# Kernel tuning notes

Hardware: AMD Instinct MI355X
Metric: run time of the kernel (lower is better)

## Reference

```python
import jax, jax.numpy as jnp
import numpy as np

R_DIM = 32
D_DIM = 64
N_AGENTS = 16
BATCH = 65536  # num_samples * N_AGENTS = 4096 * 16


def setup_inputs() -> dict:
    key = jax.random.key(0)
    kx, kl, kq, kk, kv, ko = jax.random.split(key, 6)
    x = jax.random.normal(kx, (BATCH, D_DIM, N_AGENTS), dtype=jnp.float32)
    L = jax.random.randint(kl, (BATCH, N_AGENTS, N_AGENTS), 0, 2).astype(jnp.float32)
    Aq = 0.5 * jax.random.normal(kq, (R_DIM, D_DIM), dtype=jnp.float32)
    Ak = 0.5 * jax.random.normal(kk, (R_DIM, D_DIM), dtype=jnp.float32)
    Av = 0.5 * jax.random.normal(kv, (R_DIM, D_DIM), dtype=jnp.float32)
    Ao = 0.5 * jax.random.normal(ko, (1, R_DIM), dtype=jnp.float32)
    return {"x": x, "L": L, "Aq": Aq, "Ak": Ak, "Av": Av, "Ao": Ao}


def reference(x, L, Aq, Ak, Av, Ao):
    B, d, n = x.shape
    S = B // n  # number of samples (x stacks n agents per sample)
    # numNeighbors: count of entries >= 1 in first row of L, plus 1 -> [B,1,1]
    num_neighbors = jnp.sum((L[:, 0, :] >= 1).astype(x.dtype), axis=1).reshape(-1, 1, 1) + 1.0
    # low-rank tanh-activated Q/K/V: [B, r, n]
    Q = jnp.tanh(jnp.einsum("rd,bdn->brn", Aq, x))
    K = jnp.tanh(jnp.einsum("rd,bdn->brn", Ak, x))
    V = jnp.tanh(jnp.einsum("rd,bdn->brn", Av, x))
    # attention over the rank dim r, scaled by sqrt(numNeighbors): [B, r, r]
    scores = jnp.einsum("brn,bsn->brs", Q, K) / jnp.sqrt(num_neighbors)
    attn = jax.nn.softmax(scores, axis=2)
    o = jnp.einsum("brs,bsn->brn", attn, V)  # [B, r, n]
    R = jnp.tanh(jnp.einsum("or,brn->bon", Ao, o))[:, 0, :]  # [B, n]
    R = R.reshape(S, n, n) ** 2
    eye = jnp.eye(n, dtype=R.dtype)
    Rdiag = R * (1.0 - eye)          # R with zeroed diagonal
    Rout = R * eye                    # diagonal of R only
    # Laplacian-like reconstruction: diag gets row-sum of off-diagonals, off-diag negated
    return Rout + eye * jnp.sum(Rdiag, axis=2, keepdims=True) - Rdiag
```

## Files before the change

kernel.cpp:

```cpp
#include <hip/hip_runtime.h>
#include <hip/hip_bf16.h>

#define S_SAMPLES 4096
#define NAG 16

typedef __attribute__((ext_vector_type(8))) short short8;
typedef __attribute__((ext_vector_type(4))) float f32x4;

union F8 { short8 v; unsigned u[4]; };

__device__ __forceinline__ float tanh_fast(float x) {
    float ax = fabsf(x);
    float e  = __expf(-2.0f * ax);
    float t  = (1.0f - e) * __builtin_amdgcn_rcpf(1.0f + e);
    return copysignf(t, x);
}

__device__ __forceinline__ unsigned pk2(float a, float b) {
    float2 f; f.x = a; f.y = b;
    __hip_bfloat162 h = __float22bfloat162_rn(f);
    unsigned r; __builtin_memcpy(&r, &h, 4); return r;
}

__device__ __forceinline__ short bfs(float a) {
    __hip_bfloat16 h = __float2bfloat16(a);
    short r; __builtin_memcpy(&r, &h, 2); return r;
}

__device__ __forceinline__ float4 ld4(const float* p) {
    return *reinterpret_cast<const float4*>(p);
}

#define STR 40

__global__ __launch_bounds__(256, 2) void att_mask_kernel(
    const float* __restrict__ x, const float* __restrict__ L,
    const float* __restrict__ Aq, const float* __restrict__ Ak,
    const float* __restrict__ Av, const float* __restrict__ Ao,
    float* __restrict__ out)
{
    __shared__ alignas(16) short sQ [4][32 * STR];
    __shared__ alignas(16) short sK [4][32 * STR];
    __shared__ alignas(16) short sVt[4][16 * STR];
    __shared__ alignas(16) short sAt[4][32 * STR];
    __shared__ alignas(16) float sRsq[16 * 17];

    const int tid  = threadIdx.x;
    const int lane = tid & 63;
    const int w    = tid >> 6;
    const int c4   = lane & 15;
    const int q    = lane >> 4;
    const int s_idx = blockIdx.x;

    short* qw = sQ[w];  short* kw = sK[w];  short* vtw = sVt[w];  short* atw = sAt[w];

    F8 aF[3][2][2];
    {
        const float* mats[3] = { Aq, Ak, Av };
        #pragma unroll
        for (int m = 0; m < 3; ++m)
            #pragma unroll
            for (int rh = 0; rh < 2; ++rh)
                #pragma unroll
                for (int kb = 0; kb < 2; ++kb) {
                    const float* p = mats[m] + (c4 + 16 * rh) * 64 + 32 * kb + 8 * q;
                    float4 a0 = ld4(p), a1 = ld4(p + 4);
                    aF[m][rh][kb].u[0] = pk2(a0.x, a0.y);
                    aF[m][rh][kb].u[1] = pk2(a0.z, a0.w);
                    aF[m][rh][kb].u[2] = pk2(a1.x, a1.y);
                    aF[m][rh][kb].u[3] = pk2(a1.z, a1.w);
                }
    }
    float4 ao0 = ld4(Ao + 4 * q);
    float4 ao1 = ld4(Ao + 16 + 4 * q);

    {
        int r = lane & 31, hh = lane >> 5;
        uint2 z; z.x = 0; z.y = 0;
        *reinterpret_cast<uint2*>(&qw[r * STR + 16 + 8 * hh]) = z;
        *reinterpret_cast<uint2*>(&qw[r * STR + 20 + 8 * hh]) = z;
        *reinterpret_cast<uint2*>(&kw[r * STR + 16 + 8 * hh]) = z;
        *reinterpret_cast<uint2*>(&kw[r * STR + 20 + 8 * hh]) = z;
    }

    const f32x4 zz = {0.f, 0.f, 0.f, 0.f};

    for (int t = 0; t < 4; ++t) {
        const int i_loc = w * 4 + t;
        const int b     = s_idx * NAG + i_loc;

        float lv = (lane < 16) ? L[(size_t)b * 256 + lane] : 0.0f;
        unsigned long long ball = __ballot(lv >= 1.0f);
        float scale = rsqrtf((float)(__popcll(ball) + 1));

        const float* xb = x + (size_t)b * 1024 + 128 * q + c4;
        float xv[2][8];
        #pragma unroll
        for (int kb = 0; kb < 2; ++kb)
            #pragma unroll
            for (int j = 0; j < 8; ++j)
                xv[kb][j] = xb[512 * kb + 16 * j];
        F8 bx[2];
        #pragma unroll
        for (int kb = 0; kb < 2; ++kb)
            #pragma unroll
            for (int p = 0; p < 4; ++p)
                bx[kb].u[p] = pk2(xv[kb][2 * p], xv[kb][2 * p + 1]);

        f32x4 accQ[2], accK[2], accV[2];
        #pragma unroll
        for (int rh = 0; rh < 2; ++rh) {
            accQ[rh] = __builtin_amdgcn_mfma_f32_16x16x32_bf16(aF[0][rh][0].v, bx[0].v, zz, 0, 0, 0);
            accQ[rh] = __builtin_amdgcn_mfma_f32_16x16x32_bf16(aF[0][rh][1].v, bx[1].v, accQ[rh], 0, 0, 0);
            accK[rh] = __builtin_amdgcn_mfma_f32_16x16x32_bf16(aF[1][rh][0].v, bx[0].v, zz, 0, 0, 0);
            accK[rh] = __builtin_amdgcn_mfma_f32_16x16x32_bf16(aF[1][rh][1].v, bx[1].v, accK[rh], 0, 0, 0);
            accV[rh] = __builtin_amdgcn_mfma_f32_16x16x32_bf16(aF[2][rh][0].v, bx[0].v, zz, 0, 0, 0);
            accV[rh] = __builtin_amdgcn_mfma_f32_16x16x32_bf16(aF[2][rh][1].v, bx[1].v, accV[rh], 0, 0, 0);
        }

        #pragma unroll
        for (int rh = 0; rh < 2; ++rh) {
            float tq[4], tk[4], tv[4];
            #pragma unroll
            for (int r2 = 0; r2 < 4; ++r2) {
                tq[r2] = tanh_fast(accQ[rh][r2]);
                tk[r2] = tanh_fast(accK[rh][r2]);
                tv[r2] = tanh_fast(accV[rh][r2]);
            }
            #pragma unroll
            for (int r2 = 0; r2 < 4; ++r2) {
                int r = 4 * q + r2 + 16 * rh;
                qw[r * STR + c4] = bfs(tq[r2]);
                kw[r * STR + c4] = bfs(tk[r2]);
            }
            uint2 vpk; vpk.x = pk2(tv[0], tv[1]); vpk.y = pk2(tv[2], tv[3]);
            *reinterpret_cast<uint2*>(&vtw[c4 * STR + 4 * q + 16 * rh]) = vpk;
        }
        __syncthreads();

        short8 kfrag[2], qfrag[2];
        #pragma unroll
        for (int hh = 0; hh < 2; ++hh) {
            kfrag[hh] = *reinterpret_cast<const short8*>(&kw[(c4 + 16 * hh) * STR + 8 * q]);
            qfrag[hh] = *reinterpret_cast<const short8*>(&qw[(c4 + 16 * hh) * STR + 8 * q]);
        }
        f32x4 sc[2][2];
        #pragma unroll
        for (int sh = 0; sh < 2; ++sh)
            #pragma unroll
            for (int rh2 = 0; rh2 < 2; ++rh2)
                sc[sh][rh2] = __builtin_amdgcn_mfma_f32_16x16x32_bf16(kfrag[sh], qfrag[rh2], zz, 0, 0, 0);

        #pragma unroll
        for (int rh2 = 0; rh2 < 2; ++rh2) {
            float v[8];
            #pragma unroll
            for (int sh = 0; sh < 2; ++sh)
                #pragma unroll
                for (int r2 = 0; r2 < 4; ++r2)
                    v[sh * 4 + r2] = sc[sh][rh2][r2] * scale;
            float mx = v[0];
            #pragma unroll
            for (int j2 = 1; j2 < 8; ++j2) mx = fmaxf(mx, v[j2]);
            mx = fmaxf(mx, __shfl_xor(mx, 16));
            mx = fmaxf(mx, __shfl_xor(mx, 32));
            float sum = 0.f;
            #pragma unroll
            for (int j2 = 0; j2 < 8; ++j2) { v[j2] = __expf(v[j2] - mx); sum += v[j2]; }
            sum += __shfl_xor(sum, 16);
            sum += __shfl_xor(sum, 32);
            float inv = __builtin_amdgcn_rcpf(sum);
            #pragma unroll
            for (int sh = 0; sh < 2; ++sh)
                #pragma unroll
                for (int r2 = 0; r2 < 4; ++r2)
                    sc[sh][rh2][r2] = v[sh * 4 + r2] * inv;
        }

        #pragma unroll
        for (int rh2 = 0; rh2 < 2; ++rh2)
            #pragma unroll
            for (int sh = 0; sh < 2; ++sh) {
                uint2 ap; ap.x = pk2(sc[sh][rh2][0], sc[sh][rh2][1]);
                ap.y = pk2(sc[sh][rh2][2], sc[sh][rh2][3]);
                *reinterpret_cast<uint2*>(&atw[(c4 + 16 * rh2) * STR + 4 * q + 16 * sh]) = ap;
            }
        __syncthreads();

        short8 vfrag = *reinterpret_cast<const short8*>(&vtw[c4 * STR + 8 * q]);
        f32x4 o[2];
        #pragma unroll
        for (int rh = 0; rh < 2; ++rh) {
            short8 afr = *reinterpret_cast<const short8*>(&atw[(c4 + 16 * rh) * STR + 8 * q]);
            o[rh] = __builtin_amdgcn_mfma_f32_16x16x32_bf16(afr, vfrag, zz, 0, 0, 0);
        }

        float part = 0.f;
        part = fmaf(ao0.x, o[0][0], part); part = fmaf(ao0.y, o[0][1], part);
        part = fmaf(ao0.z, o[0][2], part); part = fmaf(ao0.w, o[0][3], part);
        part = fmaf(ao1.x, o[1][0], part); part = fmaf(ao1.y, o[1][1], part);
        part = fmaf(ao1.z, o[1][2], part); part = fmaf(ao1.w, o[1][3], part);
        part += __shfl_xor(part, 16);
        part += __shfl_xor(part, 32);
        if (lane < 16) {
            float tt = tanh_fast(part);
            sRsq[i_loc * 17 + lane] = tt * tt;
        }
        __syncthreads();
    }

    {
        int i = tid >> 4, j = tid & 15;
        float rij = sRsq[i * 17 + j];
        float srow = 0.0f;
        #pragma unroll
        for (int k = 0; k < 16; ++k) srow += sRsq[i * 17 + k];
        out[(size_t)s_idx * 256 + tid] = (i == j) ? srow : -rij;
    }
}

extern "C" void kernel_launch(void* const* d_in, const int* in_sizes, int n_in,
                              void* d_out, int out_size, void* d_ws, size_t ws_size,
                              hipStream_t stream) {
    const float* x  = (const float*)d_in[0];
    const float* L  = (const float*)d_in[1];
    const float* Aq = (const float*)d_in[2];
    const float* Ak = (const float*)d_in[3];
    const float* Av = (const float*)d_in[4];
    const float* Ao = (const float*)d_in[5];
    float* out = (float*)d_out;

    dim3 grid(S_SAMPLES), block(256);
    hipLaunchKernelGGL(att_mask_kernel, grid, block, 0, stream,
                       x, L, Aq, Ak, Av, Ao, out);
}
```

Before: 399.6 us.

## Replace block barriers with wave-local LDS fences and prefetch next x/L

Each wave works on its own LDS slices, so the per-iteration block-wide __syncthreads are replaced by s_waitcnt lgkmcnt(0) fences, leaving one barrier before the final reduction. The x and L loads for the next iteration are double-buffered in registers to overlap global latency with compute. The softmax scale is folded into Q before the bf16 pack, and the max-subtraction is dropped, since the tanh-bounded scores cannot overflow exp. Risks are higher register pressure from the prefetch buffers and reliance on wave-synchronous LDS visibility without a barrier.

```diff
diff --git a/kernel.cpp b/kernel.cpp
--- a/kernel.cpp
+++ b/kernel.cpp
@@ -32,6 +32,8 @@
 }
 
 #define STR 40
+
+#define LDS_FENCE() asm volatile("s_waitcnt lgkmcnt(0)" ::: "memory")
 
 __global__ __launch_bounds__(256, 2) void att_mask_kernel(
     const float* __restrict__ x, const float* __restrict__ L,
@@ -85,27 +87,44 @@
 
     const f32x4 zz = {0.f, 0.f, 0.f, 0.f};
 
+    const int b0 = s_idx * NAG + w * 4;
+    const float* xb = x + (size_t)b0 * 1024 + 128 * q + c4;
+    const float* Lb = L + (size_t)b0 * 256 + c4;
+
+    float xv[2][16];
+    float lvb[2];
+
+    #pragma unroll
+    for (int kb = 0; kb < 2; ++kb)
+        #pragma unroll
+        for (int j = 0; j < 8; ++j)
+            xv[0][kb * 8 + j] = xb[512 * kb + 16 * j];
+    lvb[0] = (lane < 16) ? Lb[0] : 0.0f;
+
+    #pragma unroll
     for (int t = 0; t < 4; ++t) {
+        const int cur = t & 1;
+        const int nxt = cur ^ 1;
         const int i_loc = w * 4 + t;
-        const int b     = s_idx * NAG + i_loc;
-
-        float lv = (lane < 16) ? L[(size_t)b * 256 + lane] : 0.0f;
-        unsigned long long ball = __ballot(lv >= 1.0f);
+
+        unsigned long long ball = __ballot(lvb[cur] >= 1.0f);
         float scale = rsqrtf((float)(__popcll(ball) + 1));
 
-        const float* xb = x + (size_t)b * 1024 + 128 * q + c4;
-        float xv[2][8];
+        F8 bx[2];
         #pragma unroll
         for (int kb = 0; kb < 2; ++kb)
             #pragma unroll
-            for (int j = 0; j < 8; ++j)
-                xv[kb][j] = xb[512 * kb + 16 * j];
-        F8 bx[2];
-        #pragma unroll
-        for (int kb = 0; kb < 2; ++kb)
-            #pragma unroll
             for (int p = 0; p < 4; ++p)
-                bx[kb].u[p] = pk2(xv[kb][2 * p], xv[kb][2 * p + 1]);
+                bx[kb].u[p] = pk2(xv[cur][kb * 8 + 2 * p], xv[cur][kb * 8 + 2 * p + 1]);
+
+        if (t < 3) {
+            #pragma unroll
+            for (int kb = 0; kb < 2; ++kb)
+                #pragma unroll
+                for (int j = 0; j < 8; ++j)
+                    xv[nxt][kb * 8 + j] = xb[(t + 1) * 1024 + 512 * kb + 16 * j];
+            lvb[nxt] = (lane < 16) ? Lb[(t + 1) * 256] : 0.0f;
+        }
 
         f32x4 accQ[2], accK[2], accV[2];
         #pragma unroll
@@ -130,13 +149,13 @@
             #pragma unroll
             for (int r2 = 0; r2 < 4; ++r2) {
                 int r = 4 * q + r2 + 16 * rh;
-                qw[r * STR + c4] = bfs(tq[r2]);
+                qw[r * STR + c4] = bfs(tq[r2] * scale);
                 kw[r * STR + c4] = bfs(tk[r2]);
             }
             uint2 vpk; vpk.x = pk2(tv[0], tv[1]); vpk.y = pk2(tv[2], tv[3]);
             *reinterpret_cast<uint2*>(&vtw[c4 * STR + 4 * q + 16 * rh]) = vpk;
         }
-        __syncthreads();
+        LDS_FENCE();
 
         short8 kfrag[2], qfrag[2];
         #pragma unroll
@@ -151,22 +170,20 @@
             for (int rh2 = 0; rh2 < 2; ++rh2)
                 sc[sh][rh2] = __builtin_amdgcn_mfma_f32_16x16x32_bf16(kfrag[sh], qfrag[rh2], zz, 0, 0, 0);
 
+        short8 vfrag = *reinterpret_cast<const short8*>(&vtw[c4 * STR + 8 * q]);
+
         #pragma unroll
         for (int rh2 = 0; rh2 < 2; ++rh2) {
             float v[8];
+            float sum = 0.f;
             #pragma unroll
             for (int sh = 0; sh < 2; ++sh)
                 #pragma unroll
-                for (int r2 = 0; r2 < 4; ++r2)
-                    v[sh * 4 + r2] = sc[sh][rh2][r2] * scale;
-            float mx = v[0];
-            #pragma unroll
-            for (int j2 = 1; j2 < 8; ++j2) mx = fmaxf(mx, v[j2]);
-            mx = fmaxf(mx, __shfl_xor(mx, 16));
-            mx = fmaxf(mx, __shfl_xor(mx, 32));
-            float sum = 0.f;
-            #pragma unroll
-            for (int j2 = 0; j2 < 8; ++j2) { v[j2] = __expf(v[j2] - mx); sum += v[j2]; }
+                for (int r2 = 0; r2 < 4; ++r2) {
+                    float e = __expf(sc[sh][rh2][r2]);
+                    v[sh * 4 + r2] = e;
+                    sum += e;
+                }
             sum += __shfl_xor(sum, 16);
             sum += __shfl_xor(sum, 32);
             float inv = __builtin_amdgcn_rcpf(sum);
@@ -185,9 +202,8 @@
                 ap.y = pk2(sc[sh][rh2][2], sc[sh][rh2][3]);
                 *reinterpret_cast<uint2*>(&atw[(c4 + 16 * rh2) * STR + 4 * q + 16 * sh]) = ap;
             }
-        __syncthreads();
-
-        short8 vfrag = *reinterpret_cast<const short8*>(&vtw[c4 * STR + 8 * q]);
+        LDS_FENCE();
+
         f32x4 o[2];
         #pragma unroll
         for (int rh = 0; rh < 2; ++rh) {
@@ -206,8 +222,9 @@
             float tt = tanh_fast(part);
             sRsq[i_loc * 17 + lane] = tt * tt;
         }
-        __syncthreads();
-    }
+    }
+
+    __syncthreads();
 
     {
         int i = tid >> 4, j = tid & 15;
```

Result: no change. 396.2 us (-0.8%).
